# Kernel optimization log

Measured on AMD Instinct MI355X. Metric: run time of the kernel, lower is better.

Reference implementation:

```python
import jax, jax.numpy as jnp
import numpy as np
from jax import lax

B, C, H, W = 16, 64, 64, 64
K = 3                  # kernel_size
D_IN = C * K           # moe input dim = 192
D_OUT = 128            # out_channels
N_EXP = 8
TOP_K = 2
N_SHARED = 1


def setup_inputs() -> dict:
    key = jax.random.key(0)
    ks = jax.random.split(key, 7)
    x = jax.random.normal(ks[0], (B, C, H, W), dtype=jnp.float32)
    # depthwise conv: groups=C, each input channel -> K output channels
    conv_w = jax.random.normal(ks[1], (D_IN, 1, K, K), dtype=jnp.float32) * 0.1
    router_w = jax.random.normal(ks[2], (D_IN, N_EXP), dtype=jnp.float32) * 0.05
    w_experts = jax.random.normal(ks[3], (N_EXP, D_IN, D_OUT), dtype=jnp.float32) * 0.05
    b_experts = jnp.zeros((N_EXP, D_OUT), dtype=jnp.float32)
    w_shared = jax.random.normal(ks[4], (N_SHARED, D_IN, D_OUT), dtype=jnp.float32) * 0.05
    b_shared = jnp.zeros((N_SHARED, D_OUT), dtype=jnp.float32)
    return {"x": x, "conv_w": conv_w, "router_w": router_w,
            "w_experts": w_experts, "b_experts": b_experts,
            "w_shared": w_shared, "b_shared": b_shared}


def _moe_conv2d(x, conv_w, router_w, w_experts, b_experts, w_shared, b_shared):
    pad = K // 2
    # depthwise conv (B,C,H,W) -> (B, C*K, H, W)
    x_conv = lax.conv_general_dilated(
        x, conv_w, window_strides=(1, 1), padding=[(pad, pad), (pad, pad)],
        feature_group_count=C, dimension_numbers=("NCHW", "OIHW", "NCHW"))
    # flatten to token stream (B*H*W, D_IN)
    tokens = x_conv.transpose(0, 2, 3, 1).reshape(-1, D_IN)
    # router: softmax probs, top-k gating renormalized over selected experts
    logits = tokens @ router_w                       # (T, E)
    probs = jax.nn.softmax(logits, axis=-1)
    top_v, top_i = lax.top_k(probs, TOP_K)           # (T, k)
    gates = top_v / jnp.sum(top_v, axis=-1, keepdims=True)
    # all-expert outputs then gather the selected k per token
    expert_out = jnp.einsum("ti,eio->teo", tokens, w_experts) + b_experts  # (T, E, O)
    sel = jnp.take_along_axis(expert_out, top_i[:, :, None], axis=1)       # (T, k, O)
    y_flat = jnp.einsum("tk,tko->to", gates, sel)
    # shared experts applied to every token
    shared = jnp.einsum("ti,sio->tso", tokens, w_shared) + b_shared        # (T, S, O)
    y_flat = y_flat + jnp.sum(shared, axis=1)
    # back to feature map (B, O, H, W)
    return y_flat.reshape(B, H, W, D_OUT).transpose(0, 3, 1, 2)


def reference(x, conv_w, router_w, w_experts, b_experts, w_shared, b_shared):
    return _moe_conv2d(x, conv_w, router_w, w_experts, b_experts, w_shared, b_shared)
```

## Files before the change

### kernel.cpp

```cpp
#include <hip/hip_runtime.h>
#include <math.h>

#define BB   16
#define CC   64
#define DIN  192
#define DOUT 128
#define NEXP 8
#define NMAT 9
#define NTOK 65536
#define CAP  65568
#define SLABROWS 65552

#define TOKSTRIDE 200
#define LOGSTRIDE 9
#define CSTRIDE 136

typedef short bf16x8 __attribute__((ext_vector_type(8)));
typedef float f32x4  __attribute__((ext_vector_type(4)));

#define WS_TOK   0u
#define WS_WT    25165824u
#define WS_CNT   25608192u
#define WS_RT    25608256u
#define WS_RG    27706432u
#define WS_SLAB  29804608u
#define WS_TOTAL  63367232u
#define WS_TOTAL3 80148544u

__device__ __forceinline__ unsigned short f2bf(float f) {
    union { float f; unsigned u; } v; v.f = f;
    unsigned u = v.u;
    u += 0x7fffu + ((u >> 16) & 1u);
    return (unsigned short)(u >> 16);
}
__device__ __forceinline__ float bf2f(unsigned short s) {
    union { unsigned u; float f; } v; v.u = ((unsigned)s) << 16;
    return v.f;
}

__global__ __launch_bounds__(256)
void k1a_conv(const float* __restrict__ x,
              const float* __restrict__ conv_w,
              const float* __restrict__ router_w,
              const float* __restrict__ w_experts,
              const float* __restrict__ w_shared,
              unsigned short* __restrict__ tokbuf,
              unsigned short* __restrict__ wt,
              int* __restrict__ cnt,
              int* __restrict__ rowtok, float* __restrict__ rowgate)
{
    __shared__ __attribute__((aligned(16))) unsigned short tokbf[64 * TOKSTRIDE];
    __shared__ float logits[64 * LOGSTRIDE];
    __shared__ int lcnt[8];
    __shared__ int lbase[8];

    const int tid = threadIdx.x;
    const int bh  = blockIdx.x;
    const int b   = bh >> 6;
    const int h   = bh & 63;

    for (int idx = tid; idx < 64 * LOGSTRIDE; idx += 256) logits[idx] = 0.f;
    if (tid < 8) lcnt[tid] = 0;
    __syncthreads();

    {
        int idx = bh * 216 + tid;
        if (tid < 216) {
            int e = idx / 24576, rem = idx - e * 24576;
            int n = rem / DIN,  k  = rem - n * DIN;
            const float* src = (e < 8) ? (w_experts + (size_t)e * DIN * DOUT)
                                       : w_shared;
            wt[idx] = f2bf(src[k * DOUT + n]);
        }
    }

    const int   h0  = (h > 0)  ? (h - 1) : 0;
    const int   h2  = (h < 63) ? (h + 1) : 63;
    const float mh0 = (h > 0)  ? 1.f : 0.f;
    const float mh2 = (h < 63) ? 1.f : 0.f;

    const int w = tid & 63;
    const int q = __builtin_amdgcn_readfirstlane(tid >> 6);

    const int   wm  = (w == 0)  ? 0  : (w - 1);
    const int   wp  = (w == 63) ? 63 : (w + 1);
    const float mwm = (w == 0)  ? 0.f : 1.f;
    const float mwp = (w == 63) ? 0.f : 1.f;

    float lacc[8];
    #pragma unroll
    for (int e = 0; e < 8; ++e) lacc[e] = 0.f;

    const float* xb = x + (size_t)b * CC * 4096;

    #pragma unroll 2
    for (int i = 0; i < 16; ++i) {
        const int c = q * 16 + i;
        const float* xc = xb + (size_t)c * 4096;
        const float* r0 = xc + h0 * 64;
        const float* r1 = xc + h  * 64;
        const float* r2 = xc + h2 * 64;
        float x00 = r0[wm], x01 = r0[w], x02 = r0[wp];
        float x10 = r1[wm], x11 = r1[w], x12 = r1[wp];
        float x20 = r2[wm], x21 = r2[w], x22 = r2[wp];
        x00 *= mh0 * mwm; x01 *= mh0; x02 *= mh0 * mwp;
        x10 *= mwm;                    x12 *= mwp;
        x20 *= mh2 * mwm; x21 *= mh2; x22 *= mh2 * mwp;

        #pragma unroll
        for (int j = 0; j < 3; ++j) {
            const int f = 3 * c + j;
            const float* w9  = conv_w + f * 9;
            const float* rwf = router_w + f * 8;
            float acc = x00 * w9[0] + x01 * w9[1] + x02 * w9[2]
                      + x10 * w9[3] + x11 * w9[4] + x12 * w9[5]
                      + x20 * w9[6] + x21 * w9[7] + x22 * w9[8];
            tokbf[w * TOKSTRIDE + f] = f2bf(acc);
            #pragma unroll
            for (int e = 0; e < 8; ++e) lacc[e] += acc * rwf[e];
        }
    }

    #pragma unroll
    for (int e = 0; e < 8; ++e)
        atomicAdd(&logits[w * LOGSTRIDE + e], lacc[e]);
    __syncthreads();

    int e0 = 0, e1 = -1, r0k = 0, r1k = 0;
    float g0 = 0.f, g1 = 0.f;
    if (tid < 64) {
        float l[8];
        #pragma unroll
        for (int e = 0; e < 8; ++e) l[e] = logits[tid * LOGSTRIDE + e];
        float l0 = l[0];
        #pragma unroll
        for (int e = 1; e < 8; ++e) if (l[e] > l0) { l0 = l[e]; e0 = e; }
        float l1 = -INFINITY;
        #pragma unroll
        for (int e = 0; e < 8; ++e) {
            if (e == e0) continue;
            if (l[e] > l1) { l1 = l[e]; e1 = e; }
        }
        g0 = 1.f / (1.f + expf(l1 - l0));
        g1 = 1.f - g0;
        r0k = atomicAdd(&lcnt[e0], 1);
        r1k = atomicAdd(&lcnt[e1], 1);
    }
    __syncthreads();
    if (tid < 8) lbase[tid] = atomicAdd(&cnt[tid], lcnt[tid]);
    __syncthreads();
    if (tid < 64) {
        int t   = bh * 64 + tid;
        int p0i = e0 * CAP + lbase[e0] + r0k;
        int p1i = e1 * CAP + lbase[e1] + r1k;
        rowtok[p0i]  = t;
        rowgate[p0i] = g0;
        rowtok[p1i]  = t | (1 << 20);
        rowgate[p1i] = g1;
    }

    for (int idx = tid; idx < 1536; idx += 256) {
        int row = idx / 24, seg = idx - row * 24;
        *(bf16x8*)(tokbuf + (size_t)(bh * 64 + row) * 192 + seg * 8) =
            *(const bf16x8*)(tokbf + row * TOKSTRIDE + seg * 8);
    }
}

__global__ __launch_bounds__(256)
void k4_all(const unsigned short* __restrict__ tokbuf,
            const unsigned short* __restrict__ wt,
            const float* __restrict__ b_experts,
            const float* __restrict__ b_shared,
            const int* __restrict__ cnt,
            const int* __restrict__ rowtok, const float* __restrict__ rowgate,
            unsigned short* __restrict__ slab)
{
    __shared__ __attribute__((aligned(16))) unsigned short atile[2][16 * TOKSTRIDE];
    __shared__ __attribute__((aligned(16))) unsigned short ctile[2][16 * CSTRIDE];
    __shared__ int   stok[2][16];
    __shared__ float sgate[2][16];

    const int tid  = threadIdx.x;
    int e, jb, jstep;
    if (blockIdx.x < 2048) { e = blockIdx.x >> 8; jb = blockIdx.x & 255; jstep = 256; }
    else                   { e = 8; jb = blockIdx.x - 2048; jstep = 1024; }
    const bool dense = (e == 8);

    const int wave = tid >> 6;
    const int lane = tid & 63;
    const int m16  = lane & 15, quad = lane >> 4;
    const int o0   = (wave * 2 + 0) * 16 + m16;
    const int o1   = (wave * 2 + 1) * 16 + m16;

    const unsigned short* wb = wt + (size_t)e * DOUT * DIN;
    bf16x8 bfr0[6], bfr1[6];
    #pragma unroll
    for (int ks = 0; ks < 6; ++ks) {
        bfr0[ks] = *(const bf16x8*)(wb + (size_t)o0 * DIN + ks * 32 + quad * 8);
        bfr1[ks] = *(const bf16x8*)(wb + (size_t)o1 * DIN + ks * 32 + quad * 8);
    }
    const float be0 = dense ? b_shared[o0] : b_experts[e * DOUT + o0];
    const float be1 = dense ? b_shared[o1] : b_experts[e * DOUT + o1];

    const int cnt_e  = dense ? NTOK : cnt[e];
    const int ntiles = (cnt_e + 15) >> 4;
    const int*   rt = rowtok  + e * CAP;
    const float* rg = rowgate + e * CAP;

    const int r0i = tid / 24,         s0i = tid - r0i * 24;
    const int r1i = (tid + 256) / 24, s1i = (tid + 256) - r1i * 24;
    const bool has1 = (tid + 256) < 384;

    #define FETCH_RAW(r) (dense ? ((r) | (2 << 20)) : (((r) < cnt_e) ? rt[r] : NTOK))
    #define FETCH_G(r)   (dense ? 1.f : (((r) < cnt_e) ? rg[r] : 0.f))

    if (jb < ntiles) {
        int base = jb * 16;
        if (tid < 16) {
            stok[0][tid]  = FETCH_RAW(base + tid);
            sgate[0][tid] = FETCH_G(base + tid);
        }
        {
            int rawa = FETCH_RAW(base + r0i);
            *(bf16x8*)&atile[0][r0i * TOKSTRIDE + s0i * 8] =
                *(const bf16x8*)(tokbuf + (size_t)(rawa & 0x1FFFF) * 192 + s0i * 8);
            if (has1) {
                int rawb = FETCH_RAW(base + r1i);
                *(bf16x8*)&atile[0][r1i * TOKSTRIDE + s1i * 8] =
                    *(const bf16x8*)(tokbuf + (size_t)(rawb & 0x1FFFF) * 192 + s1i * 8);
            }
        }
    }
    __syncthreads();

    int buf = 0;
    for (int j = jb; j < ntiles; j += jstep, buf ^= 1) {
        const int jn = j + jstep;
        const bool more = (jn < ntiles);

        bf16x8 nx0 = {0,0,0,0,0,0,0,0}, nx1 = {0,0,0,0,0,0,0,0};
        int nmt = NTOK; float nmg = 0.f;
        if (more) {
            int base = jn * 16;
            if (tid < 16) { nmt = FETCH_RAW(base + tid); nmg = FETCH_G(base + tid); }
            int rawa = FETCH_RAW(base + r0i);
            nx0 = *(const bf16x8*)(tokbuf + (size_t)(rawa & 0x1FFFF) * 192 + s0i * 8);
            if (has1) {
                int rawb = FETCH_RAW(base + r1i);
                nx1 = *(const bf16x8*)(tokbuf + (size_t)(rawb & 0x1FFFF) * 192 + s1i * 8);
            }
        }

        bf16x8 a[6];
        #pragma unroll
        for (int ks = 0; ks < 6; ++ks)
            a[ks] = *(const bf16x8*)&atile[buf][m16 * TOKSTRIDE + ks * 32 + quad * 8];

        f32x4 acc0 = {0.f, 0.f, 0.f, 0.f};
        f32x4 acc1 = {0.f, 0.f, 0.f, 0.f};
        #pragma unroll
        for (int ks = 0; ks < 6; ++ks) {
            acc0 = __builtin_amdgcn_mfma_f32_16x16x32_bf16(a[ks], bfr0[ks], acc0, 0, 0, 0);
            acc1 = __builtin_amdgcn_mfma_f32_16x16x32_bf16(a[ks], bfr1[ks], acc1, 0, 0, 0);
        }

        #pragma unroll
        for (int i = 0; i < 4; ++i) {
            int   row = quad * 4 + i;
            float g   = sgate[buf][row];
            ctile[buf][row * CSTRIDE + o0] = f2bf(g * (acc0[i] + be0));
            ctile[buf][row * CSTRIDE + o1] = f2bf(g * (acc1[i] + be1));
        }

        if (more) {
            if (tid < 16) { stok[buf ^ 1][tid] = nmt; sgate[buf ^ 1][tid] = nmg; }
            *(bf16x8*)&atile[buf ^ 1][r0i * TOKSTRIDE + s0i * 8] = nx0;
            if (has1) *(bf16x8*)&atile[buf ^ 1][r1i * TOKSTRIDE + s1i * 8] = nx1;
        }
        __syncthreads();

        {
            int row = tid >> 4, chk = tid & 15;
            int raw = stok[buf][row];
            int t    = raw & 0x1FFFF;
            int slot = raw >> 20;
            *(bf16x8*)(slab + (size_t)slot * SLABROWS * DOUT
                            + (size_t)t * DOUT + chk * 8) =
                *(const bf16x8*)&ctile[buf][row * CSTRIDE + chk * 8];
        }
    }
    #undef FETCH_RAW
    #undef FETCH_G
}

__global__ __launch_bounds__(256)
void k3_combine(const unsigned short* __restrict__ slab,
                float* __restrict__ out)
{
    __shared__ float out_lds[32 * 129];

    const int tid = threadIdx.x;
    const int bid = blockIdx.x;
    const int bh  = bid >> 1;
    const int wh  = bid & 1;
    const int b   = bh >> 6;
    const int h   = bh & 63;
    const int t0  = bh * 64 + wh * 32;

    const unsigned short* s0 = slab;
    const unsigned short* s1 = slab + (size_t)SLABROWS * DOUT;
    const unsigned short* s2 = slab + (size_t)2 * SLABROWS * DOUT;

    #pragma unroll
    for (int it = 0; it < 2; ++it) {
        int idx = it * 256 + tid;
        int tl = idx >> 4, chk = idx & 15;
        size_t gt = (size_t)t0 + tl;
        bf16x8 v0 = *(const bf16x8*)(s0 + gt * DOUT + chk * 8);
        bf16x8 v1 = *(const bf16x8*)(s1 + gt * DOUT + chk * 8);
        bf16x8 v2 = *(const bf16x8*)(s2 + gt * DOUT + chk * 8);
        float* dst = &out_lds[tl * 129 + chk * 8];
        #pragma unroll
        for (int q = 0; q < 8; ++q)
            dst[q] = bf2f((unsigned short)v0[q]) + bf2f((unsigned short)v1[q])
                   + bf2f((unsigned short)v2[q]);
    }
    __syncthreads();

    float* outp = out + ((size_t)b * DOUT) * 4096 + h * 64 + wh * 32;
    for (int idx = tid; idx < 32 * DOUT; idx += 256) {
        int wloc = idx & 31, o = idx >> 5;
        outp[(size_t)o * 4096 + wloc] = out_lds[wloc * 129 + o];
    }
}

__global__ __launch_bounds__(256)
void k3_shared(const unsigned short* __restrict__ tokbuf,
               const unsigned short* __restrict__ wt,
               const unsigned short* __restrict__ slab,
               const float* __restrict__ b_shared,
               float* __restrict__ out)
{
    __shared__ float out_lds[32 * 129];

    const int tid  = threadIdx.x;
    const int bid  = blockIdx.x;
    const int bh   = bid >> 1;
    const int wh   = bid & 1;
    const int b    = bh >> 6;
    const int h    = bh & 63;
    const int wave = tid >> 6, lane = tid & 63;
    const int mt   = wave >> 1, nh = wave & 1;
    const int m16  = lane & 15, quad = lane >> 4;
    const int t0   = bh * 64 + wh * 32;

    bf16x8 pv0[2], pv1[2];
    {
        const unsigned short* s0 = slab;
        const unsigned short* s1 = slab + (size_t)SLABROWS * DOUT;
        #pragma unroll
        for (int it = 0; it < 2; ++it) {
            int idx = it * 256 + tid;
            int tl = idx >> 4, chk = idx & 15;
            size_t gt = (size_t)t0 + tl;
            pv0[it] = *(const bf16x8*)(s0 + gt * DOUT + chk * 8);
            pv1[it] = *(const bf16x8*)(s1 + gt * DOUT + chk * 8);
        }
    }

    const unsigned short* ap =
        tokbuf + (size_t)(t0 + mt * 16 + m16) * 192 + quad * 8;
    bf16x8 a[6];
    #pragma unroll
    for (int ks = 0; ks < 6; ++ks) a[ks] = *(const bf16x8*)(ap + ks * 32);

    const unsigned short* wsh = wt + (size_t)8 * DOUT * DIN;

    bf16x8 bcur[6], bnxt[6];
    {
        int o = (nh * 4 + 0) * 16 + m16;
        const unsigned short* bp = wsh + (size_t)o * DIN + quad * 8;
        #pragma unroll
        for (int ks = 0; ks < 6; ++ks) bcur[ks] = *(const bf16x8*)(bp + ks * 32);
    }
    #pragma unroll
    for (int nb2 = 0; nb2 < 4; ++nb2) {
        if (nb2 < 3) {
            int on = (nh * 4 + nb2 + 1) * 16 + m16;
            const unsigned short* bp = wsh + (size_t)on * DIN + quad * 8;
            #pragma unroll
            for (int ks = 0; ks < 6; ++ks) bnxt[ks] = *(const bf16x8*)(bp + ks * 32);
        }
        int o = (nh * 4 + nb2) * 16 + m16;
        f32x4 acc = {0.f, 0.f, 0.f, 0.f};
        #pragma unroll
        for (int ks = 0; ks < 6; ++ks)
            acc = __builtin_amdgcn_mfma_f32_16x16x32_bf16(a[ks], bcur[ks], acc, 0, 0, 0);
        float bs = b_shared[o];
        #pragma unroll
        for (int i = 0; i < 4; ++i) {
            int tloc = mt * 16 + quad * 4 + i;
            out_lds[tloc * 129 + o] = acc[i] + bs;
        }
        #pragma unroll
        for (int ks = 0; ks < 6; ++ks) bcur[ks] = bnxt[ks];
    }
    __syncthreads();

    #pragma unroll
    for (int it = 0; it < 2; ++it) {
        int idx = it * 256 + tid;
        int tl = idx >> 4, chk = idx & 15;
        float* dst = &out_lds[tl * 129 + chk * 8];
        #pragma unroll
        for (int q = 0; q < 8; ++q)
            dst[q] += bf2f((unsigned short)pv0[it][q])
                    + bf2f((unsigned short)pv1[it][q]);
    }
    __syncthreads();

    float* outp = out + ((size_t)b * DOUT) * 4096 + h * 64 + wh * 32;
    for (int idx = tid; idx < 32 * DOUT; idx += 256) {
        int wloc = idx & 31, o = idx >> 5;
        outp[(size_t)o * 4096 + wloc] = out_lds[wloc * 129 + o];
    }
}

#define OUTSTRIDE 129
#define MAXROWS 320
#define MAXTILES 20

__global__ __launch_bounds__(256)
void moe_conv2d_mfma(const float* __restrict__ x,
                     const float* __restrict__ conv_w,
                     const float* __restrict__ router_w,
                     const unsigned short* __restrict__ wt,
                     const float* __restrict__ b_experts,
                     const float* __restrict__ b_shared,
                     float* __restrict__ out)
{
    __shared__ __attribute__((aligned(16))) unsigned short tokbf[64 * TOKSTRIDE];
    __shared__ float out_lds[64 * OUTSTRIDE];
    __shared__ float rw[DIN * NEXP];
    __shared__ float logits[64 * LOGSTRIDE];
    __shared__ float sg0[64], sg1[64];
    __shared__ int   se0[64], se1[64];
    __shared__ int   rowtok[MAXROWS];
    __shared__ float rowgate[MAXROWS];
    __shared__ int   cbuf[NMAT];
    __shared__ int   tilexp[MAXTILES], tilebase[MAXTILES];
    __shared__ int   ntiles_s;

    const int tid = threadIdx.x;
    const int bh  = blockIdx.x;
    const int b   = bh >> 6;
    const int h   = bh & 63;

    for (int idx = tid; idx < DIN * NEXP; idx += 256) rw[idx] = router_w[idx];
    for (int idx = tid; idx < 64 * LOGSTRIDE; idx += 256) logits[idx] = 0.f;
    __syncthreads();
    {
        const int w  = tid & 63;
        const int fq = tid >> 6;
        float lacc[8];
        #pragma unroll
        for (int e = 0; e < 8; ++e) lacc[e] = 0.f;
        for (int i = 0; i < 48; ++i) {
            int f = i * 4 + fq;
            int c = f / 3;
            const float* wp    = conv_w + f * 9;
            const float* xbase = x + ((size_t)(b * 64 + c) * 64) * 64;
            float acc = 0.f;
            #pragma unroll
            for (int kh = 0; kh < 3; ++kh) {
                int hh = h + kh - 1;
                if (hh < 0 || hh > 63) continue;
                const float* xrow = xbase + hh * 64;
                #pragma unroll
                for (int kw = 0; kw < 3; ++kw) {
                    int ww = w + kw - 1;
                    if (ww < 0 || ww > 63) continue;
                    acc += xrow[ww] * wp[kh * 3 + kw];
                }
            }
            tokbf[w * TOKSTRIDE + f] = f2bf(acc);
            const float* rwf = rw + f * 8;
            #pragma unroll
            for (int e = 0; e < 8; ++e) lacc[e] += acc * rwf[e];
        }
        #pragma unroll
        for (int e = 0; e < 8; ++e)
            atomicAdd(&logits[w * LOGSTRIDE + e], lacc[e]);
    }
    __syncthreads();
    if (tid < 64) {
        int w = tid;
        float l[8];
        #pragma unroll
        for (int e = 0; e < 8; ++e) l[e] = logits[w * LOGSTRIDE + e];
        int e0 = 0; float l0 = l[0];
        #pragma unroll
        for (int e = 1; e < 8; ++e) if (l[e] > l0) { l0 = l[e]; e0 = e; }
        int e1 = -1; float l1 = -INFINITY;
        #pragma unroll
        for (int e = 0; e < 8; ++e) {
            if (e == e0) continue;
            if (l[e] > l1) { l1 = l[e]; e1 = e; }
        }
        float g0 = 1.f / (1.f + expf(l1 - l0));
        sg0[w] = g0; sg1[w] = 1.f - g0;
        se0[w] = e0; se1[w] = e1;
    }
    __syncthreads();
    for (int idx = tid; idx < 64 * DOUT; idx += 256) {
        int t = idx >> 7, o = idx & 127;
        out_lds[t * OUTSTRIDE + o] = b_shared[o]
            + sg0[t] * b_experts[se0[t] * DOUT + o]
            + sg1[t] * b_experts[se1[t] * DOUT + o];
    }
    if (tid < 8) {
        int c = 0;
        for (int t = 0; t < 64; ++t) c += (se0[t] == tid) + (se1[t] == tid);
        cbuf[tid] = c;
    } else if (tid == 8) cbuf[8] = 64;
    __syncthreads();
    if (tid < NMAT) {
        int e = tid;
        int start = 0, tb = 0;
        for (int e2 = 0; e2 < e; ++e2) {
            int ce = cbuf[e2];
            int tl = (ce + 15) >> 4;
            start += tl << 4; tb += tl;
        }
        int ce = cbuf[e];
        int tl = (ce + 15) >> 4;
        for (int j = 0; j < tl; ++j) { tilexp[tb + j] = e; tilebase[tb + j] = start + (j << 4); }
        if (e == 8) ntiles_s = tb + tl;
        int j = 0;
        if (e < 8) {
            for (int t = 0; t < 64; ++t) {
                if (se0[t] == e) { rowtok[start + j] = t; rowgate[start + j] = sg0[t]; ++j; }
                if (se1[t] == e) { rowtok[start + j] = t; rowgate[start + j] = sg1[t]; ++j; }
            }
        } else {
            for (int t = 0; t < 64; ++t) { rowtok[start + j] = t; rowgate[start + j] = 1.f; ++j; }
        }
        for (; j < (tl << 4); ++j) { rowtok[start + j] = 0; rowgate[start + j] = 0.f; }
    }
    __syncthreads();
    {
        const int wave = tid >> 6;
        const int lane = tid & 63;
        const int m16  = lane & 15;
        const int quad = lane >> 4;
        const int nt   = ntiles_s;
        for (int ti = wave; ti < nt; ti += 4) {
            int e    = tilexp[ti];
            int base = tilebase[ti];
            int tA = rowtok[base + m16];
            bf16x8 a[6];
            #pragma unroll
            for (int ks = 0; ks < 6; ++ks)
                a[ks] = *(const bf16x8*)(tokbf + tA * TOKSTRIDE + ks * 32 + quad * 8);
            int st[4]; float sgt[4];
            #pragma unroll
            for (int i2 = 0; i2 < 4; ++i2) {
                int r = base + quad * 4 + i2;
                st[i2] = rowtok[r]; sgt[i2] = rowgate[r];
            }
            const unsigned short* we = wt + (size_t)e * DOUT * DIN;
            for (int n = 0; n < 8; ++n) {
                const unsigned short* wp = we + (size_t)(n * 16 + m16) * DIN + quad * 8;
                f32x4 acc = {0.f, 0.f, 0.f, 0.f};
                #pragma unroll
                for (int ks = 0; ks < 6; ++ks) {
                    bf16x8 bfr2 = *(const bf16x8*)(wp + ks * 32);
                    acc = __builtin_amdgcn_mfma_f32_16x16x32_bf16(a[ks], bfr2, acc, 0, 0, 0);
                }
                int ncol = n * 16 + m16;
                #pragma unroll
                for (int i2 = 0; i2 < 4; ++i2)
                    atomicAdd(&out_lds[st[i2] * OUTSTRIDE + ncol], sgt[i2] * acc[i2]);
            }
        }
    }
    __syncthreads();
    {
        float* outp = out + (((size_t)b * DOUT) * 64 + h) * 64;
        for (int idx = tid; idx < 64 * DOUT; idx += 256) {
            int w = idx & 63, o = idx >> 6;
            outp[(size_t)o * 4096 + w] = out_lds[w * OUTSTRIDE + o];
        }
    }
}

__global__ __launch_bounds__(256)
void prep_weights_only(const float* __restrict__ w_experts,
                       const float* __restrict__ w_shared,
                       unsigned short* __restrict__ wt)
{
    int e = blockIdx.x;
    const float* src = (e < 8) ? (w_experts + (size_t)e * DIN * DOUT) : w_shared;
    unsigned short* dst = wt + (size_t)e * DOUT * DIN;
    for (int idx = threadIdx.x; idx < DOUT * DIN; idx += 256) {
        int n = idx / DIN, k = idx - n * DIN;
        dst[idx] = f2bf(src[k * DOUT + n]);
    }
}

extern "C" void kernel_launch(void* const* d_in, const int* in_sizes, int n_in,
                              void* d_out, int out_size, void* d_ws, size_t ws_size,
                              hipStream_t stream)
{
    const float* x         = (const float*)d_in[0];
    const float* conv_w    = (const float*)d_in[1];
    const float* router_w  = (const float*)d_in[2];
    const float* w_experts = (const float*)d_in[3];
    const float* b_experts = (const float*)d_in[4];
    const float* w_shared  = (const float*)d_in[5];
    const float* b_shared  = (const float*)d_in[6];
    float* out = (float*)d_out;
    char* ws = (char*)d_ws;

    if (ws_size >= WS_TOTAL) {
        unsigned short* tokbuf  = (unsigned short*)(ws + WS_TOK);
        unsigned short* wt      = (unsigned short*)(ws + WS_WT);
        int*            cnt     = (int*)(ws + WS_CNT);
        int*            rowtok  = (int*)(ws + WS_RT);
        float*          rowgate = (float*)(ws + WS_RG);
        unsigned short* slab    = (unsigned short*)(ws + WS_SLAB);

        hipMemsetAsync(cnt, 0, 16 * sizeof(int), stream);
        k1a_conv<<<dim3(1024), dim3(256), 0, stream>>>(
            x, conv_w, router_w, w_experts, w_shared,
            tokbuf, wt, cnt, rowtok, rowgate);
        if (ws_size >= WS_TOTAL3) {
            k4_all<<<dim3(3072), dim3(256), 0, stream>>>(
                tokbuf, wt, b_experts, b_shared, cnt, rowtok, rowgate, slab);
            k3_combine<<<dim3(2048), dim3(256), 0, stream>>>(slab, out);
        } else {
            k4_all<<<dim3(2048), dim3(256), 0, stream>>>(
                tokbuf, wt, b_experts, b_shared, cnt, rowtok, rowgate, slab);
            k3_shared<<<dim3(2048), dim3(256), 0, stream>>>(
                tokbuf, wt, slab, b_shared, out);
        }
    } else {
        unsigned short* wt = (unsigned short*)ws;
        prep_weights_only<<<dim3(NMAT), dim3(256), 0, stream>>>(w_experts, w_shared, wt);
        moe_conv2d_mfma<<<dim3(1024), dim3(256), 0, stream>>>(
            x, conv_w, router_w, wt, b_experts, b_shared, out);
    }
}
```

Measured before the change: 159.7 us.

## Fold shared-expert weights and bias into each routed expert's weights

The top-2 gates are renormalised to sum to one, so the shared expert can be added into every routed expert's weight matrix and bias (W_e + W_s, b_e + b_s). Only the 8 expert matrices are packed now, and the dense shared-expert GEMM blocks are dropped from k4_all. The combine kernel now sums two slabs instead of three, and the fallback k3_shared path is removed. This removes a full-token GEMM plus one slab write and read. In exchange, the shared contribution depends on the gates summing exactly to one, and the sum is rounded to bf16 once per expert copy.

Result: faster. 149.0 us (-6.7%).

```diff
diff --git a/kernel.cpp b/kernel.cpp
--- a/kernel.cpp
+++ b/kernel.cpp
@@ -64,13 +64,12 @@
     __syncthreads();
 
     {
-        int idx = bh * 216 + tid;
-        if (tid < 216) {
+        int idx = bh * 192 + tid;
+        if (tid < 192) {
             int e = idx / 24576, rem = idx - e * 24576;
             int n = rem / DIN,  k  = rem - n * DIN;
-            const float* src = (e < 8) ? (w_experts + (size_t)e * DIN * DOUT)
-                                       : w_shared;
-            wt[idx] = f2bf(src[k * DOUT + n]);
+            wt[idx] = f2bf(w_experts[(size_t)e * 24576 + k * DOUT + n]
+                           + w_shared[k * DOUT + n]);
         }
     }
 
@@ -181,10 +180,9 @@
     __shared__ float sgate[2][16];
 
     const int tid  = threadIdx.x;
-    int e, jb, jstep;
-    if (blockIdx.x < 2048) { e = blockIdx.x >> 8; jb = blockIdx.x & 255; jstep = 256; }
-    else                   { e = 8; jb = blockIdx.x - 2048; jstep = 1024; }
-    const bool dense = (e == 8);
+    const int e    = blockIdx.x >> 8;
+    const int jb   = blockIdx.x & 255;
+    const int jstep = 256;
 
     const int wave = tid >> 6;
     const int lane = tid & 63;
@@ -199,10 +197,10 @@
         bfr0[ks] = *(const bf16x8*)(wb + (size_t)o0 * DIN + ks * 32 + quad * 8);
         bfr1[ks] = *(const bf16x8*)(wb + (size_t)o1 * DIN + ks * 32 + quad * 8);
     }
-    const float be0 = dense ? b_shared[o0] : b_experts[e * DOUT + o0];
-    const float be1 = dense ? b_shared[o1] : b_experts[e * DOUT + o1];
-
-    const int cnt_e  = dense ? NTOK : cnt[e];
+    const float be0 = b_experts[e * DOUT + o0] + b_shared[o0];
+    const float be1 = b_experts[e * DOUT + o1] + b_shared[o1];
+
+    const int cnt_e  = cnt[e];
     const int ntiles = (cnt_e + 15) >> 4;
     const int*   rt = rowtok  + e * CAP;
     const float* rg = rowgate + e * CAP;
@@ -211,8 +209,8 @@
     const int r1i = (tid + 256) / 24, s1i = (tid + 256) - r1i * 24;
     const bool has1 = (tid + 256) < 384;
 
-    #define FETCH_RAW(r) (dense ? ((r) | (2 << 20)) : (((r) < cnt_e) ? rt[r] : NTOK))
-    #define FETCH_G(r)   (dense ? 1.f : (((r) < cnt_e) ? rg[r] : 0.f))
+    #define FETCH_RAW(r) (((r) < cnt_e) ? rt[r] : NTOK)
+    #define FETCH_G(r)   (((r) < cnt_e) ? rg[r] : 0.f)
 
     if (jb < ntiles) {
         int base = jb * 16;
@@ -309,7 +307,6 @@
 
     const unsigned short* s0 = slab;
     const unsigned short* s1 = slab + (size_t)SLABROWS * DOUT;
-    const unsigned short* s2 = slab + (size_t)2 * SLABROWS * DOUT;
 
     #pragma unroll
     for (int it = 0; it < 2; ++it) {
@@ -318,104 +315,10 @@
         size_t gt = (size_t)t0 + tl;
         bf16x8 v0 = *(const bf16x8*)(s0 + gt * DOUT + chk * 8);
         bf16x8 v1 = *(const bf16x8*)(s1 + gt * DOUT + chk * 8);
-        bf16x8 v2 = *(const bf16x8*)(s2 + gt * DOUT + chk * 8);
         float* dst = &out_lds[tl * 129 + chk * 8];
         #pragma unroll
         for (int q = 0; q < 8; ++q)
-            dst[q] = bf2f((unsigned short)v0[q]) + bf2f((unsigned short)v1[q])
-                   + bf2f((unsigned short)v2[q]);
-    }
-    __syncthreads();
-
-    float* outp = out + ((size_t)b * DOUT) * 4096 + h * 64 + wh * 32;
-    for (int idx = tid; idx < 32 * DOUT; idx += 256) {
-        int wloc = idx & 31, o = idx >> 5;
-        outp[(size_t)o * 4096 + wloc] = out_lds[wloc * 129 + o];
-    }
-}
-
-__global__ __launch_bounds__(256)
-void k3_shared(const unsigned short* __restrict__ tokbuf,
-               const unsigned short* __restrict__ wt,
-               const unsigned short* __restrict__ slab,
-               const float* __restrict__ b_shared,
-               float* __restrict__ out)
-{
-    __shared__ float out_lds[32 * 129];
-
-    const int tid  = threadIdx.x;
-    const int bid  = blockIdx.x;
-    const int bh   = bid >> 1;
-    const int wh   = bid & 1;
-    const int b    = bh >> 6;
-    const int h    = bh & 63;
-    const int wave = tid >> 6, lane = tid & 63;
-    const int mt   = wave >> 1, nh = wave & 1;
-    const int m16  = lane & 15, quad = lane >> 4;
-    const int t0   = bh * 64 + wh * 32;
-
-    bf16x8 pv0[2], pv1[2];
-    {
-        const unsigned short* s0 = slab;
-        const unsigned short* s1 = slab + (size_t)SLABROWS * DOUT;
-        #pragma unroll
-        for (int it = 0; it < 2; ++it) {
-            int idx = it * 256 + tid;
-            int tl = idx >> 4, chk = idx & 15;
-            size_t gt = (size_t)t0 + tl;
-            pv0[it] = *(const bf16x8*)(s0 + gt * DOUT + chk * 8);
-            pv1[it] = *(const bf16x8*)(s1 + gt * DOUT + chk * 8);
-        }
-    }
-
-    const unsigned short* ap =
-        tokbuf + (size_t)(t0 + mt * 16 + m16) * 192 + quad * 8;
-    bf16x8 a[6];
-    #pragma unroll
-    for (int ks = 0; ks < 6; ++ks) a[ks] = *(const bf16x8*)(ap + ks * 32);
-
-    const unsigned short* wsh = wt + (size_t)8 * DOUT * DIN;
-
-    bf16x8 bcur[6], bnxt[6];
-    {
-        int o = (nh * 4 + 0) * 16 + m16;
-        const unsigned short* bp = wsh + (size_t)o * DIN + quad * 8;
-        #pragma unroll
-        for (int ks = 0; ks < 6; ++ks) bcur[ks] = *(const bf16x8*)(bp + ks * 32);
-    }
-    #pragma unroll
-    for (int nb2 = 0; nb2 < 4; ++nb2) {
-        if (nb2 < 3) {
-            int on = (nh * 4 + nb2 + 1) * 16 + m16;
-            const unsigned short* bp = wsh + (size_t)on * DIN + quad * 8;
-            #pragma unroll
-            for (int ks = 0; ks < 6; ++ks) bnxt[ks] = *(const bf16x8*)(bp + ks * 32);
-        }
-        int o = (nh * 4 + nb2) * 16 + m16;
-        f32x4 acc = {0.f, 0.f, 0.f, 0.f};
-        #pragma unroll
-        for (int ks = 0; ks < 6; ++ks)
-            acc = __builtin_amdgcn_mfma_f32_16x16x32_bf16(a[ks], bcur[ks], acc, 0, 0, 0);
-        float bs = b_shared[o];
-        #pragma unroll
-        for (int i = 0; i < 4; ++i) {
-            int tloc = mt * 16 + quad * 4 + i;
-            out_lds[tloc * 129 + o] = acc[i] + bs;
-        }
-        #pragma unroll
-        for (int ks = 0; ks < 6; ++ks) bcur[ks] = bnxt[ks];
-    }
-    __syncthreads();
-
-    #pragma unroll
-    for (int it = 0; it < 2; ++it) {
-        int idx = it * 256 + tid;
-        int tl = idx >> 4, chk = idx & 15;
-        float* dst = &out_lds[tl * 129 + chk * 8];
-        #pragma unroll
-        for (int q = 0; q < 8; ++q)
-            dst[q] += bf2f((unsigned short)pv0[it][q])
-                    + bf2f((unsigned short)pv1[it][q]);
+            dst[q] = bf2f((unsigned short)v0[q]) + bf2f((unsigned short)v1[q]);
     }
     __syncthreads();
 
@@ -634,16 +537,9 @@
         k1a_conv<<<dim3(1024), dim3(256), 0, stream>>>(
             x, conv_w, router_w, w_experts, w_shared,
             tokbuf, wt, cnt, rowtok, rowgate);
-        if (ws_size >= WS_TOTAL3) {
-            k4_all<<<dim3(3072), dim3(256), 0, stream>>>(
-                tokbuf, wt, b_experts, b_shared, cnt, rowtok, rowgate, slab);
-            k3_combine<<<dim3(2048), dim3(256), 0, stream>>>(slab, out);
-        } else {
-            k4_all<<<dim3(2048), dim3(256), 0, stream>>>(
-                tokbuf, wt, b_experts, b_shared, cnt, rowtok, rowgate, slab);
-            k3_shared<<<dim3(2048), dim3(256), 0, stream>>>(
-                tokbuf, wt, slab, b_shared, out);
-        }
+        k4_all<<<dim3(2048), dim3(256), 0, stream>>>(
+            tokbuf, wt, b_experts, b_shared, cnt, rowtok, rowgate, slab);
+        k3_combine<<<dim3(2048), dim3(256), 0, stream>>>(slab, out);
     } else {
         unsigned short* wt = (unsigned short*)ws;
         prep_weights_only<<<dim3(NMAT), dim3(256), 0, stream>>>(w_experts, w_shared, wt);
```
